# Kernel tuning notes

Hardware: AMD Instinct MI355X
Metric: run time of the kernel (lower is better)

## Reference

```python
import jax, jax.numpy as jnp
import numpy as np

B, N, T = 16, 1024, 100
SPEED = 0.05  # diffusion_speed


def make_Qt():
    # Qt[t-1] = [[1-p, p], [p, 1-p]], p = 0.5*(1 - (1-2*speed)^t), t in [1, T]
    ts = jnp.arange(1, T + 1, dtype=jnp.float32)
    flip = 0.5 * (1.0 - (1.0 - 2.0 * SPEED) ** ts)
    nf = 1.0 - flip
    return jnp.stack([jnp.stack([nf, flip], -1), jnp.stack([flip, nf], -1)], -2)  # [T,2,2]


def setup_inputs() -> dict:
    key = jax.random.key(0)
    k1, k2, k3 = jax.random.split(key, 3)
    adj_start = jax.random.randint(k1, (B, N, N), 0, 2, dtype=jnp.int32)
    t = jax.random.randint(k2, (B,), 0, T, dtype=jnp.int32)
    # denoise_fn output stand-in: per-edge Bernoulli probs in (0,1)
    q_approx = jax.random.uniform(k3, (B * N * N,), dtype=jnp.float32, minval=1e-4, maxval=1.0 - 1e-4)
    return {"adj_start": adj_start, "t": t, "q_approx": q_approx, "Qt": make_Qt()}


def reference(adj_start, t, q_approx, Qt):
    b = adj_start.shape[0]
    bidx = jnp.arange(b)[:, None, None]                      # [B,1,1]

    # ---- forward_diffusion: q = Qt[t][adj_start]; adj_t ~ Categorical(q) ----
    Q_ev = Qt[t]                                             # [B,2,2]
    q_fwd = Q_ev[bidx, adj_start]                            # [B,N,N,2]
    adj_t = jax.random.categorical(jax.random.key(42), jnp.log(q_fwd), axis=-1).astype(jnp.int32)

    # ---- backward_diffusion: posterior q(x_{t-1} | x_t, x_0) ----
    likelihood = Qt[0][adj_t]                                # [B,N,N,2]
    prior = Qt[t - 1][bidx, adj_start]                       # [B,N,N,2]
    evidence = Q_ev[bidx, adj_start, adj_t]                  # [B,N,N]
    q_backward = likelihood * prior / evidence[..., None]    # [B,N,N,2]
    q_target = q_backward[..., 0].reshape(-1)                # [B*N*N]

    # ---- loss: BCE(q_approx, q_target), torch-style log clamping ----
    logp = jnp.clip(jnp.log(q_approx), -100.0)
    log1mp = jnp.clip(jnp.log1p(-q_approx), -100.0)
    loss = -jnp.mean(q_target * logp + (1.0 - q_target) * log1mp)
    return loss
```

## Files before the change

kernel.cpp:

```cpp
#include <hip/hip_runtime.h>
#include <stdint.h>


#define T_STEPS 100
#define NE 16777216
#define EPT 8
#define NBLK (NE / EPT / 256)

struct BTab {
  uint32_t thr0, thr1;
  float qt00, qt01, qt10, qt11;
};

__device__ __forceinline__ BTab make_tab(const float* __restrict__ Qt, int tb) {
  int tm1 = (tb == 0) ? (T_STEPS - 1) : (tb - 1);
  float e00 = Qt[tb * 4 + 0], e01 = Qt[tb * 4 + 1];
  float e10 = Qt[tb * 4 + 2], e11 = Qt[tb * 4 + 3];
  float p0 = Qt[tm1 * 4 + 0];
  float p1 = Qt[tm1 * 4 + 2];
  float L00 = Qt[0];
  float L10 = Qt[2];
  BTab t;
  t.thr0 = (uint32_t)((double)e01 * 4294967296.0);
  t.thr1 = (uint32_t)((double)e11 * 4294967296.0);
  t.qt00 = L00 * p0 / e00;
  t.qt01 = L10 * p0 / e01;
  t.qt10 = L00 * p1 / e10;
  t.qt11 = L10 * p1 / e11;
  return t;
}

__device__ __forceinline__ uint32_t mmhash(uint32_t h) {
  h ^= h >> 16; h *= 0x85ebca6bu;
  h ^= h >> 13; h *= 0xc2b2ae35u;
  h ^= h >> 16;
  return h;
}

__device__ __forceinline__ float elem_term(uint32_t e, int a, const BTab& bt,
                                           float q) {
  uint32_t thr = a ? bt.thr1 : bt.thr0;
  bool adj1 = mmhash(e) < thr;
  float qt = a ? (adj1 ? bt.qt11 : bt.qt10)
               : (adj1 ? bt.qt01 : bt.qt00);
  float logp  = fmaxf(__logf(q), -100.0f);
  float log1m = fmaxf(__logf(1.0f - q), -100.0f);
  return fmaf(qt, logp - log1m, log1m);
}

__global__ __launch_bounds__(256) void diff_loss_kernel(
    const int* __restrict__ adj, const int* __restrict__ tvec,
    const float* __restrict__ qap, const float* __restrict__ Qt,
    double* __restrict__ ws) {
  const int tid = blockIdx.x * 256 + threadIdx.x;
  const uint32_t e0 = (uint32_t)tid * EPT;
  const int b = blockIdx.x >> 9;
  const BTab bt = make_tab(Qt, tvec[b]);

  const int4*   a4 = (const int4*)(adj + e0);
  const float4* q4 = (const float4*)(qap + e0);
  int4   aA = a4[0], aB = a4[1];
  float4 qA = q4[0], qB = q4[1];

  float s = elem_term(e0 + 0u, aA.x, bt, qA.x);
  s += elem_term(e0 + 1u, aA.y, bt, qA.y);
  s += elem_term(e0 + 2u, aA.z, bt, qA.z);
  s += elem_term(e0 + 3u, aA.w, bt, qA.w);
  s += elem_term(e0 + 4u, aB.x, bt, qB.x);
  s += elem_term(e0 + 5u, aB.y, bt, qB.y);
  s += elem_term(e0 + 6u, aB.z, bt, qB.z);
  s += elem_term(e0 + 7u, aB.w, bt, qB.w);

  double d = (double)s;
  #pragma unroll
  for (int off = 32; off > 0; off >>= 1)
    d += __shfl_down(d, off, 64);

  __shared__ double red[4];
  const int lane = threadIdx.x & 63;
  const int wv = threadIdx.x >> 6;
  if (lane == 0) red[wv] = d;
  __syncthreads();
  if (threadIdx.x == 0) {
    double tot = red[0] + red[1] + red[2] + red[3];
    unsafeAtomicAdd(&ws[blockIdx.x & 63], tot);
  }
}

__global__ void finalize_k(const double* __restrict__ ws,
                           float* __restrict__ out) {
  if (threadIdx.x == 0 && blockIdx.x == 0) {
    double s = 0.0;
    #pragma unroll
    for (int i = 0; i < 64; ++i) s += ws[i];
    out[0] = (float)(-s / (double)NE);
  }
}

extern "C" void kernel_launch(void* const* d_in, const int* in_sizes, int n_in,
                              void* d_out, int out_size, void* d_ws, size_t ws_size,
                              hipStream_t stream) {
  const int*   adj = (const int*)d_in[0];
  const int*   tv  = (const int*)d_in[1];
  const float* qap = (const float*)d_in[2];
  const float* Qt  = (const float*)d_in[3];
  double* ws = (double*)d_ws;

  hipMemsetAsync(ws, 0, 64 * sizeof(double), stream);
  diff_loss_kernel<<<NBLK, 256, 0, stream>>>(adj, tv, qap, Qt, ws);
  finalize_k<<<1, 64, 0, stream>>>(ws, (float*)d_out);
}
```

Measured before the change: 164.5 us.

## Process 16 elements per thread and use per-wave atomics without shared reduction

Doubles the elements handled per thread, halving the grid, and issues all four 16-byte loads per array up front for more memory-level parallelism. The wave reduction now runs in float instead of double, and each wave's lane 0 atomically adds to the 64-slot workspace directly, so the shared-memory stage and block barrier are gone. The cost is four times as many global atomics per block, plus slightly less precise partial sums and more register pressure.

```diff
diff --git a/kernel.cpp b/kernel.cpp
--- a/kernel.cpp
+++ b/kernel.cpp
@@ -4,7 +4,7 @@
 
 #define T_STEPS 100
 #define NE 16777216
-#define EPT 8
+#define EPT 16
 #define NBLK (NE / EPT / 256)
 
 struct BTab {
@@ -54,44 +54,43 @@
     double* __restrict__ ws) {
   const int tid = blockIdx.x * 256 + threadIdx.x;
   const uint32_t e0 = (uint32_t)tid * EPT;
-  const int b = blockIdx.x >> 9;
+  const int b = blockIdx.x >> 8;
   const BTab bt = make_tab(Qt, tvec[b]);
 
   const int4*   a4 = (const int4*)(adj + e0);
   const float4* q4 = (const float4*)(qap + e0);
-  int4   aA = a4[0], aB = a4[1];
-  float4 qA = q4[0], qB = q4[1];
+  int4   aV[4];
+  float4 qV[4];
+#pragma unroll
+  for (int i = 0; i < 4; ++i) aV[i] = a4[i];
+#pragma unroll
+  for (int i = 0; i < 4; ++i) qV[i] = q4[i];
 
-  float s = elem_term(e0 + 0u, aA.x, bt, qA.x);
-  s += elem_term(e0 + 1u, aA.y, bt, qA.y);
-  s += elem_term(e0 + 2u, aA.z, bt, qA.z);
-  s += elem_term(e0 + 3u, aA.w, bt, qA.w);
-  s += elem_term(e0 + 4u, aB.x, bt, qB.x);
-  s += elem_term(e0 + 5u, aB.y, bt, qB.y);
-  s += elem_term(e0 + 6u, aB.z, bt, qB.z);
-  s += elem_term(e0 + 7u, aB.w, bt, qB.w);
+  float s = 0.0f;
+#pragma unroll
+  for (int i = 0; i < 4; ++i) {
+    uint32_t eb = e0 + 4u * (uint32_t)i;
+    s += elem_term(eb + 0u, aV[i].x, bt, qV[i].x);
+    s += elem_term(eb + 1u, aV[i].y, bt, qV[i].y);
+    s += elem_term(eb + 2u, aV[i].z, bt, qV[i].z);
+    s += elem_term(eb + 3u, aV[i].w, bt, qV[i].w);
+  }
 
-  double d = (double)s;
-  #pragma unroll
+#pragma unroll
   for (int off = 32; off > 0; off >>= 1)
-    d += __shfl_down(d, off, 64);
+    s += __shfl_down(s, off, 64);
 
-  __shared__ double red[4];
   const int lane = threadIdx.x & 63;
   const int wv = threadIdx.x >> 6;
-  if (lane == 0) red[wv] = d;
-  __syncthreads();
-  if (threadIdx.x == 0) {
-    double tot = red[0] + red[1] + red[2] + red[3];
-    unsafeAtomicAdd(&ws[blockIdx.x & 63], tot);
-  }
+  if (lane == 0)
+    unsafeAtomicAdd(&ws[((blockIdx.x << 2) | wv) & 63], (double)s);
 }
 
 __global__ void finalize_k(const double* __restrict__ ws,
                            float* __restrict__ out) {
   if (threadIdx.x == 0 && blockIdx.x == 0) {
     double s = 0.0;
-    #pragma unroll
+#pragma unroll
     for (int i = 0; i < 64; ++i) s += ws[i];
     out[0] = (float)(-s / (double)NE);
   }
```

Result: slower. 172.4 us (+4.8%).
